# Optimization experiments

Hardware: AMD Instinct MI355X
Metric: run time of the kernel (lower is better)

The kernel has to match this reference:

```python
import jax, jax.numpy as jnp
import numpy as np

ALPHA = 0.1

def setup_inputs() -> dict:
    key = jax.random.key(0)
    k1, k2, k3, k4 = jax.random.split(key, 4)
    B, T, D_IN, H, R = 32, 2048, 128, 512, 2
    x = jax.random.normal(k1, (B, T, D_IN), dtype=jnp.float32)
    m = jax.random.normal(k2, (H, R), dtype=jnp.float32) / np.sqrt(H)
    n = jax.random.normal(k3, (H, R), dtype=jnp.float32) / np.sqrt(H)
    I = jax.random.normal(k4, (H, D_IN), dtype=jnp.float32) / np.sqrt(H)
    return {"x": x, "m": m, "n": n, "I": I}

def reference(x, m, n, I):
    # x: [B, T, D_in]; m,n: [H, R]; I: [H, D_in]
    B = x.shape[0]
    H = m.shape[0]
    J = m @ n.T  # [H, H] low-rank recurrent matrix, as in the torch module
    # Precompute input projection for all timesteps: (I @ x_t^T)^T == x_t @ I^T
    x_proj = jnp.einsum('btd,hd->bth', x, I)  # [B, T, H]
    h0 = jnp.zeros((B, H), dtype=x.dtype)

    def step(h, xp_t):
        dh = -h + jnp.tanh(h) @ J.T + xp_t  # (J @ tanh(h)^T)^T == tanh(h) @ J^T
        h = h + ALPHA * dh
        return h, h

    _, hiddens = jax.lax.scan(step, h0, jnp.swapaxes(x_proj, 0, 1))  # [T, B, H]
    return jnp.swapaxes(hiddens, 0, 1)  # [B, T, H]
```

## Files before the change

### kernel.cpp

```cpp
#include <hip/hip_runtime.h>


#define ALPHA 0.1f
typedef float v2 __attribute__((ext_vector_type(2)));
typedef short s16x8 __attribute__((ext_vector_type(8)));
typedef float f32x4 __attribute__((ext_vector_type(4)));
typedef unsigned short u16x8 __attribute__((ext_vector_type(8)));
typedef __attribute__((address_space(1))) ushort g_u16;
typedef __attribute__((address_space(3))) ushort l_u16;

__device__ __forceinline__ ushort f2bf(float x) {
  uint u = __float_as_uint(x);
  return (ushort)((u + 0x7FFFu + ((u >> 16) & 1u)) >> 16);
}
__device__ __forceinline__ float bf2f(ushort h) {
  return __uint_as_float(((uint)h) << 16);
}
__device__ __forceinline__ int swz(int row, int k) {
  return row * 128 + (k ^ ((row & 7) << 3));
}

#define MFMA __builtin_amdgcn_mfma_f32_16x16x32_bf16

__global__ __launch_bounds__(256)
void to_bf16_swz(const float* __restrict__ X, const float* __restrict__ Iw,
                 ushort* __restrict__ Xh, ushort* __restrict__ Ih) {
  const int b = blockIdx.x;
  const float* src;
  ushort* dh;
  int gid;
  if (b < 4096) {
    src = X; dh = Xh; gid = b * 256 + threadIdx.x;
  } else {
    src = Iw; dh = Ih; gid = (b - 4096) * 256 + threadIdx.x;
  }
  const int row = gid >> 4;
  const int k0 = (gid & 15) * 8;
  const float4* p = (const float4*)(src + (size_t)row * 128 + k0);
  float4 a = p[0], bq = p[1];
  float v[8] = {a.x, a.y, a.z, a.w, bq.x, bq.y, bq.z, bq.w};
  u16x8 hi;
#pragma unroll
  for (int i = 0; i < 8; ++i) hi[i] = f2bf(v[i]);
  const int ks = k0 ^ ((row & 7) << 3);
  *(u16x8*)&dh[(size_t)row * 128 + ks] = hi;
}

__global__ __launch_bounds__(256, 4)
void xproj_gemm2(const ushort* __restrict__ Xh, const ushort* __restrict__ Ih,
                 ushort* __restrict__ C) {
  __shared__ ushort Ahs[64 * 128];
  __shared__ ushort Bhs[64 * 128];

  const int u = blockIdx.x;
  const int m0 = ((u & 7) * 128 + (u >> 6)) * 64;
  const int n0 = ((u >> 3) & 7) * 64;

  const int id = threadIdx.x;
  const int lane = id & 63;
  const int wid = id >> 6;

  {
    const int half = (wid & 1) * 32;
    const ushort* g;
    ushort* l;
    if (wid < 2) { g = Xh + (size_t)(m0 + half) * 128; l = Ahs + half * 128; }
    else         { g = Ih + (size_t)(n0 + half) * 128; l = Bhs + half * 128; }
    g += lane * 8;
#pragma unroll
    for (int i = 0; i < 8; ++i)
      __builtin_amdgcn_global_load_lds((const g_u16*)(g + i * 512),
                                       (l_u16*)(l + i * 512), 16, 0, 0);
  }
  __syncthreads();

  const int wr = (wid >> 1) * 32;
  const int wc = (wid & 1) * 32;
  const int fr = lane & 15;
  const int fk = (lane >> 4) * 8;

  f32x4 acc[2][2] = {};

#pragma unroll
  for (int kk = 0; kk < 4; ++kk) {
    const int kb = kk * 32 + fk;
    s16x8 ahi[2], bhi[2];
#pragma unroll
    for (int i = 0; i < 2; ++i)
      ahi[i] = *(const s16x8*)&Ahs[swz(wr + i * 16 + fr, kb)];
#pragma unroll
    for (int jn = 0; jn < 2; ++jn)
      bhi[jn] = *(const s16x8*)&Bhs[swz(wc + jn * 16 + fr, kb)];
#pragma unroll
    for (int i = 0; i < 2; ++i)
#pragma unroll
      for (int jn = 0; jn < 2; ++jn)
        acc[i][jn] = MFMA(ahi[i], bhi[jn], acc[i][jn], 0, 0, 0);
  }

#pragma unroll
  for (int i = 0; i < 2; ++i)
#pragma unroll
    for (int jn = 0; jn < 2; ++jn) {
      int r0 = m0 + wr + i * 16 + (lane >> 4) * 4;
      int c0 = n0 + wc + jn * 16 + (lane & 15);
#pragma unroll
      for (int t = 0; t < 4; ++t)
        C[(size_t)(r0 + t) * 512 + c0] = f2bf(acc[i][jn][t]);
    }
}

__global__ __launch_bounds__(256, 2)
void xproj_gemm_fused(const float* __restrict__ X, const float* __restrict__ Iw,
                      float* __restrict__ C) {
  __shared__ ushort Ahs[64 * 128];
  __shared__ ushort Bhs[64 * 128];

  const int u = blockIdx.x;
  const int m0 = ((u & 7) * 128 + (u >> 6)) * 64;
  const int n0 = ((u >> 3) & 7) * 64;
  const int id = threadIdx.x;

#pragma unroll
  for (int j = 0; j < 8; ++j) {
    int f = id + 256 * j;
    int row = f >> 5, c4 = f & 31;
    int k0 = 4 * c4;
    float4 a4 = *(const float4*)(X + (size_t)(m0 + row) * 128 + k0);
    float4 b4 = *(const float4*)(Iw + (size_t)(n0 + row) * 128 + k0);
    int sa = swz(row, k0);
    *(ushort4*)&Ahs[sa] =
        make_ushort4(f2bf(a4.x), f2bf(a4.y), f2bf(a4.z), f2bf(a4.w));
    *(ushort4*)&Bhs[sa] =
        make_ushort4(f2bf(b4.x), f2bf(b4.y), f2bf(b4.z), f2bf(b4.w));
  }
  __syncthreads();

  const int lane = id & 63;
  const int wid = id >> 6;
  const int wr = (wid >> 1) * 32;
  const int wc = (wid & 1) * 32;
  const int fr = lane & 15;
  const int fk = (lane >> 4) * 8;

  f32x4 acc[2][2] = {};
#pragma unroll
  for (int kk = 0; kk < 4; ++kk) {
    const int kb = kk * 32 + fk;
    s16x8 ahi[2], bhi[2];
#pragma unroll
    for (int i = 0; i < 2; ++i)
      ahi[i] = *(const s16x8*)&Ahs[swz(wr + i * 16 + fr, kb)];
#pragma unroll
    for (int jn = 0; jn < 2; ++jn)
      bhi[jn] = *(const s16x8*)&Bhs[swz(wc + jn * 16 + fr, kb)];
#pragma unroll
    for (int i = 0; i < 2; ++i)
#pragma unroll
      for (int jn = 0; jn < 2; ++jn)
        acc[i][jn] = MFMA(ahi[i], bhi[jn], acc[i][jn], 0, 0, 0);
  }
#pragma unroll
  for (int i = 0; i < 2; ++i)
#pragma unroll
    for (int jn = 0; jn < 2; ++jn) {
      int r0 = m0 + wr + i * 16 + (lane >> 4) * 4;
      int c0 = n0 + wc + jn * 16 + (lane & 15);
#pragma unroll
      for (int t = 0; t < 4; ++t)
        C[(size_t)(r0 + t) * 512 + c0] = acc[i][jn][t];
    }
}

#define DPP_STEP(v, ctrl)                                                     \
  ((v) + __int_as_float(__builtin_amdgcn_update_dpp(                          \
             0, __float_as_int(v), (ctrl), 0xf, 0xf, true)))

__device__ __forceinline__ float wave_sum63(float v) {
  v = DPP_STEP(v, 0x111);
  v = DPP_STEP(v, 0x112);
  v = DPP_STEP(v, 0x114);
  v = DPP_STEP(v, 0x118);
  v = DPP_STEP(v, 0x142);
  v = DPP_STEP(v, 0x143);
  return v;
}

struct ScanState {
  v2 m0v[4], m1v[4], n0v[4], n1v[4], hv[4];
};

__device__ __forceinline__ void scan_init(ScanState& S, const float* mw,
                                          const float* nw, int base) {
  const float2* mp = (const float2*)mw;
  const float2* np = (const float2*)nw;
#pragma unroll
  for (int p = 0; p < 4; ++p) {
    float2 ma = mp[base + 2 * p], mb = mp[base + 2 * p + 1];
    float2 na = np[base + 2 * p], nb = np[base + 2 * p + 1];
    S.m0v[p] = (v2){ma.x, mb.x};
    S.m1v[p] = (v2){ma.y, mb.y};
    S.n0v[p] = (v2){ALPHA * na.x, ALPHA * nb.x};
    S.n1v[p] = (v2){ALPHA * na.y, ALPHA * nb.y};
    S.hv[p] = (v2){0.f, 0.f};
  }
}

__device__ __forceinline__ void scan_step(ScanState& S, u16x8 xr) {
  const v2 TC0 = (v2){-5.70498872745e-3f, -5.70498872745e-3f};
  const v2 TC1 = (v2){2.06390887954e-2f, 2.06390887954e-2f};
  const v2 TC2 = (v2){-5.37397155531e-2f, -5.37397155531e-2f};
  const v2 TC3 = (v2){1.33314422036e-1f, 1.33314422036e-1f};
  const v2 TC4 = (v2){-3.33332819422e-1f, -3.33332819422e-1f};
  const v2 CLO = (v2){-1.15f, -1.15f};
  const v2 CHI = (v2){1.15f, 1.15f};
  const v2 K9 = (v2){1.f - ALPHA, 1.f - ALPHA};
  const v2 KA = (v2){ALPHA, ALPHA};

  v2 xpv[4];
#pragma unroll
  for (int p = 0; p < 4; ++p)
    xpv[p] = (v2){bf2f(xr[2 * p]), bf2f(xr[2 * p + 1])};

  v2 p0 = (v2){0.f, 0.f}, p1 = (v2){0.f, 0.f};
#pragma unroll
  for (int p = 0; p < 4; ++p) {
    v2 xc = __builtin_elementwise_min(
        __builtin_elementwise_max(S.hv[p], CLO), CHI);
    v2 z = xc * xc;
    v2 q = __builtin_elementwise_fma(z, TC0, TC1);
    q = __builtin_elementwise_fma(z, q, TC2);
    q = __builtin_elementwise_fma(z, q, TC3);
    q = __builtin_elementwise_fma(z, q, TC4);
    v2 th = __builtin_elementwise_fma(xc * z, q, xc);
    p0 = __builtin_elementwise_fma(th, S.n0v[p], p0);
    p1 = __builtin_elementwise_fma(th, S.n1v[p], p1);
  }
  float s0 = wave_sum63(p0.x + p0.y);
  float s1 = wave_sum63(p1.x + p1.y);
  s0 = __int_as_float(__builtin_amdgcn_readlane(__float_as_int(s0), 63));
  s1 = __int_as_float(__builtin_amdgcn_readlane(__float_as_int(s1), 63));
  v2 s0v = (v2){s0, s0}, s1v = (v2){s1, s1};
#pragma unroll
  for (int p = 0; p < 4; ++p) {
    v2 d = __builtin_elementwise_fma(s0v, S.m0v[p], s1v * S.m1v[p]);
    S.hv[p] = __builtin_elementwise_fma(
        K9, S.hv[p], __builtin_elementwise_fma(KA, xpv[p], d));
  }
}

#define CS 32
#define CW 96

__global__ __launch_bounds__(64, 1)
void rnn_scan_chunk(const float* __restrict__ mw, const float* __restrict__ nw,
                    const ushort* __restrict__ xp, float* __restrict__ out) {
  const int b = blockIdx.x;
  const int c = blockIdx.y;
  const int base = threadIdx.x * 8;

  ScanState S;
  scan_init(S, mw, nw, base);

  const ushort* xrow = xp + (size_t)b * 2048 * 512 + base;
  float* orow = out + (size_t)b * 2048 * 512 + base;

  const int t1 = c * CS;
  int t0 = t1 - CW;
  if (t0 < 0) t0 = 0;
  const int t2 = t1 + CS;
  const int warm_blocks = (t1 - t0) >> 3;
  const int tot_blocks = (t2 - t0) >> 3;

  u16x8 ra[8];
#pragma unroll
  for (int u = 0; u < 8; ++u)
    ra[u] = *(const u16x8*)(xrow + (size_t)(t0 + u) * 512);

  for (int bb = 0; bb < tot_blocks; ++bb) {
    const int tb = t0 + bb * 8;
    const bool refill = (bb + 1 < tot_blocks);
    const bool dostore = (bb >= warm_blocks);
#pragma unroll
    for (int u = 0; u < 8; ++u) {
      u16x8 xr = ra[u];
      if (refill)
        ra[u] = *(const u16x8*)(xrow + (size_t)(tb + 8 + u) * 512);
      scan_step(S, xr);
      if (dostore) {
        f32x4 o0 = {S.hv[0].x, S.hv[0].y, S.hv[1].x, S.hv[1].y};
        f32x4 o1 = {S.hv[2].x, S.hv[2].y, S.hv[3].x, S.hv[3].y};
        __builtin_nontemporal_store(o0, (f32x4*)(orow + (size_t)(tb + u) * 512));
        __builtin_nontemporal_store(o1, (f32x4*)(orow + (size_t)(tb + u) * 512 + 4));
      }
    }
  }
}

__device__ __forceinline__ void scan_step_f32(ScanState& S, float4 xa, float4 xb) {
  u16x8 dummy;
  const v2 TC0 = (v2){-5.70498872745e-3f, -5.70498872745e-3f};
  const v2 TC1 = (v2){2.06390887954e-2f, 2.06390887954e-2f};
  const v2 TC2 = (v2){-5.37397155531e-2f, -5.37397155531e-2f};
  const v2 TC3 = (v2){1.33314422036e-1f, 1.33314422036e-1f};
  const v2 TC4 = (v2){-3.33332819422e-1f, -3.33332819422e-1f};
  const v2 CLO = (v2){-1.15f, -1.15f};
  const v2 CHI = (v2){1.15f, 1.15f};
  const v2 K9 = (v2){1.f - ALPHA, 1.f - ALPHA};
  const v2 KA = (v2){ALPHA, ALPHA};
  (void)dummy;
  v2 xpv[4] = {(v2){xa.x, xa.y}, (v2){xa.z, xa.w},
               (v2){xb.x, xb.y}, (v2){xb.z, xb.w}};
  v2 p0 = (v2){0.f, 0.f}, p1 = (v2){0.f, 0.f};
#pragma unroll
  for (int p = 0; p < 4; ++p) {
    v2 xc = __builtin_elementwise_min(
        __builtin_elementwise_max(S.hv[p], CLO), CHI);
    v2 z = xc * xc;
    v2 q = __builtin_elementwise_fma(z, TC0, TC1);
    q = __builtin_elementwise_fma(z, q, TC2);
    q = __builtin_elementwise_fma(z, q, TC3);
    q = __builtin_elementwise_fma(z, q, TC4);
    v2 th = __builtin_elementwise_fma(xc * z, q, xc);
    p0 = __builtin_elementwise_fma(th, S.n0v[p], p0);
    p1 = __builtin_elementwise_fma(th, S.n1v[p], p1);
  }
  float s0 = wave_sum63(p0.x + p0.y);
  float s1 = wave_sum63(p1.x + p1.y);
  s0 = __int_as_float(__builtin_amdgcn_readlane(__float_as_int(s0), 63));
  s1 = __int_as_float(__builtin_amdgcn_readlane(__float_as_int(s1), 63));
  v2 s0v = (v2){s0, s0}, s1v = (v2){s1, s1};
#pragma unroll
  for (int p = 0; p < 4; ++p) {
    v2 d = __builtin_elementwise_fma(s0v, S.m0v[p], s1v * S.m1v[p]);
    S.hv[p] = __builtin_elementwise_fma(
        K9, S.hv[p], __builtin_elementwise_fma(KA, xpv[p], d));
  }
}

__global__ __launch_bounds__(64, 1)
void rnn_scan_serial(const float* __restrict__ mw, const float* __restrict__ nw,
                     float* __restrict__ out) {
  const int b = blockIdx.x;
  const int base = threadIdx.x * 8;
  ScanState S;
  scan_init(S, mw, nw, base);
  float* row = out + (size_t)b * 2048 * 512 + base;

  float4 ra[8], rb[8];
#pragma unroll
  for (int u = 0; u < 8; ++u) {
    ra[u] = *(const float4*)(row + (size_t)u * 512);
    rb[u] = *(const float4*)(row + (size_t)u * 512 + 4);
  }
  for (int bb = 0; bb < 256; ++bb) {
    const int tb = bb * 8;
    const bool refill = (bb + 1 < 256);
#pragma unroll
    for (int u = 0; u < 8; ++u) {
      float4 xa = ra[u], xb = rb[u];
      if (refill) {
        ra[u] = *(const float4*)(row + (size_t)(tb + 8 + u) * 512);
        rb[u] = *(const float4*)(row + (size_t)(tb + 8 + u) * 512 + 4);
      }
      scan_step_f32(S, xa, xb);
      *(float4*)(row + (size_t)(tb + u) * 512) =
          make_float4(S.hv[0].x, S.hv[0].y, S.hv[1].x, S.hv[1].y);
      *(float4*)(row + (size_t)(tb + u) * 512 + 4) =
          make_float4(S.hv[2].x, S.hv[2].y, S.hv[3].x, S.hv[3].y);
    }
  }
}

extern "C" void kernel_launch(void* const* d_in, const int* in_sizes, int n_in,
                              void* d_out, int out_size, void* d_ws, size_t ws_size,
                              hipStream_t stream) {
  const float* x  = (const float*)d_in[0];
  const float* mw = (const float*)d_in[1];
  const float* nw = (const float*)d_in[2];
  const float* Iw = (const float*)d_in[3];
  float* out = (float*)d_out;

  const size_t xp_bytes = 32ull * 2048ull * 512ull * 2ull;

  if (ws_size >= xp_bytes) {
    ushort* xp = (ushort*)d_ws;
    ushort* Xh = (ushort*)out;
    ushort* Ih = Xh + 65536ull * 128ull;
    to_bf16_swz<<<4128, 256, 0, stream>>>(x, Iw, Xh, Ih);
    xproj_gemm2<<<8192, 256, 0, stream>>>(Xh, Ih, xp);
    rnn_scan_chunk<<<dim3(32, 2048 / CS), 64, 0, stream>>>(mw, nw, xp, out);
  } else {
    xproj_gemm_fused<<<8192, 256, 0, stream>>>(x, Iw, out);
    rnn_scan_serial<<<32, 64, 0, stream>>>(mw, nw, out);
  }
}
```

Baseline: 242.3 us.

## Interleave two independent scan chunks per wave to hide serial latency

Each 64-thread block now processes two adjacent time chunks, A and B, of the same batch row in lockstep. Their independent recurrences are interleaved so the DPP reduction and tanh-polynomial latency of one chain can overlap with the other, and the grid shrinks from 64 to 32 chunk-blocks per batch. The cost is double the register state and fewer waves in flight. Chunk A runs fewer steps than chunk B and is masked off for its last blocks, but it still executes those redundant steps.

Result: slower. 278.0 us (+14.7%).

```diff
diff --git a/kernel.cpp b/kernel.cpp
--- a/kernel.cpp
+++ b/kernel.cpp
@@ -186,12 +186,12 @@
   return v;
 }
 
-struct ScanState {
-  v2 m0v[4], m1v[4], n0v[4], n1v[4], hv[4];
+struct ScanState2 {
+  v2 m0v[4], m1v[4], n0v[4], n1v[4], hA[4], hB[4];
 };
 
-__device__ __forceinline__ void scan_init(ScanState& S, const float* mw,
-                                          const float* nw, int base) {
+__device__ __forceinline__ void scan_init2(ScanState2& S, const float* mw,
+                                           const float* nw, int base) {
   const float2* mp = (const float2*)mw;
   const float2* np = (const float2*)nw;
 #pragma unroll
@@ -202,11 +202,12 @@
     S.m1v[p] = (v2){ma.y, mb.y};
     S.n0v[p] = (v2){ALPHA * na.x, ALPHA * nb.x};
     S.n1v[p] = (v2){ALPHA * na.y, ALPHA * nb.y};
-    S.hv[p] = (v2){0.f, 0.f};
-  }
-}
-
-__device__ __forceinline__ void scan_step(ScanState& S, u16x8 xr) {
+    S.hA[p] = (v2){0.f, 0.f};
+    S.hB[p] = (v2){0.f, 0.f};
+  }
+}
+
+__device__ __forceinline__ void scan_step2(ScanState2& S, u16x8 xrA, u16x8 xrB) {
   const v2 TC0 = (v2){-5.70498872745e-3f, -5.70498872745e-3f};
   const v2 TC1 = (v2){2.06390887954e-2f, 2.06390887954e-2f};
   const v2 TC2 = (v2){-5.37397155531e-2f, -5.37397155531e-2f};
@@ -217,35 +218,55 @@
   const v2 K9 = (v2){1.f - ALPHA, 1.f - ALPHA};
   const v2 KA = (v2){ALPHA, ALPHA};
 
-  v2 xpv[4];
-#pragma unroll
-  for (int p = 0; p < 4; ++p)
-    xpv[p] = (v2){bf2f(xr[2 * p]), bf2f(xr[2 * p + 1])};
-
-  v2 p0 = (v2){0.f, 0.f}, p1 = (v2){0.f, 0.f};
-#pragma unroll
-  for (int p = 0; p < 4; ++p) {
-    v2 xc = __builtin_elementwise_min(
-        __builtin_elementwise_max(S.hv[p], CLO), CHI);
-    v2 z = xc * xc;
-    v2 q = __builtin_elementwise_fma(z, TC0, TC1);
-    q = __builtin_elementwise_fma(z, q, TC2);
-    q = __builtin_elementwise_fma(z, q, TC3);
-    q = __builtin_elementwise_fma(z, q, TC4);
-    v2 th = __builtin_elementwise_fma(xc * z, q, xc);
-    p0 = __builtin_elementwise_fma(th, S.n0v[p], p0);
-    p1 = __builtin_elementwise_fma(th, S.n1v[p], p1);
-  }
-  float s0 = wave_sum63(p0.x + p0.y);
-  float s1 = wave_sum63(p1.x + p1.y);
-  s0 = __int_as_float(__builtin_amdgcn_readlane(__float_as_int(s0), 63));
-  s1 = __int_as_float(__builtin_amdgcn_readlane(__float_as_int(s1), 63));
-  v2 s0v = (v2){s0, s0}, s1v = (v2){s1, s1};
-#pragma unroll
-  for (int p = 0; p < 4; ++p) {
-    v2 d = __builtin_elementwise_fma(s0v, S.m0v[p], s1v * S.m1v[p]);
-    S.hv[p] = __builtin_elementwise_fma(
-        K9, S.hv[p], __builtin_elementwise_fma(KA, xpv[p], d));
+  v2 xpA[4], xpB[4];
+#pragma unroll
+  for (int p = 0; p < 4; ++p) {
+    xpA[p] = (v2){bf2f(xrA[2 * p]), bf2f(xrA[2 * p + 1])};
+    xpB[p] = (v2){bf2f(xrB[2 * p]), bf2f(xrB[2 * p + 1])};
+  }
+
+  v2 p0A = (v2){0.f, 0.f}, p1A = (v2){0.f, 0.f};
+  v2 p0B = (v2){0.f, 0.f}, p1B = (v2){0.f, 0.f};
+#pragma unroll
+  for (int p = 0; p < 4; ++p) {
+    v2 xcA = __builtin_elementwise_min(
+        __builtin_elementwise_max(S.hA[p], CLO), CHI);
+    v2 xcB = __builtin_elementwise_min(
+        __builtin_elementwise_max(S.hB[p], CLO), CHI);
+    v2 zA = xcA * xcA, zB = xcB * xcB;
+    v2 qA = __builtin_elementwise_fma(zA, TC0, TC1);
+    v2 qB = __builtin_elementwise_fma(zB, TC0, TC1);
+    qA = __builtin_elementwise_fma(zA, qA, TC2);
+    qB = __builtin_elementwise_fma(zB, qB, TC2);
+    qA = __builtin_elementwise_fma(zA, qA, TC3);
+    qB = __builtin_elementwise_fma(zB, qB, TC3);
+    qA = __builtin_elementwise_fma(zA, qA, TC4);
+    qB = __builtin_elementwise_fma(zB, qB, TC4);
+    v2 thA = __builtin_elementwise_fma(xcA * zA, qA, xcA);
+    v2 thB = __builtin_elementwise_fma(xcB * zB, qB, xcB);
+    p0A = __builtin_elementwise_fma(thA, S.n0v[p], p0A);
+    p1A = __builtin_elementwise_fma(thA, S.n1v[p], p1A);
+    p0B = __builtin_elementwise_fma(thB, S.n0v[p], p0B);
+    p1B = __builtin_elementwise_fma(thB, S.n1v[p], p1B);
+  }
+  float s0A = wave_sum63(p0A.x + p0A.y);
+  float s1A = wave_sum63(p1A.x + p1A.y);
+  float s0B = wave_sum63(p0B.x + p0B.y);
+  float s1B = wave_sum63(p1B.x + p1B.y);
+  s0A = __int_as_float(__builtin_amdgcn_readlane(__float_as_int(s0A), 63));
+  s1A = __int_as_float(__builtin_amdgcn_readlane(__float_as_int(s1A), 63));
+  s0B = __int_as_float(__builtin_amdgcn_readlane(__float_as_int(s0B), 63));
+  s1B = __int_as_float(__builtin_amdgcn_readlane(__float_as_int(s1B), 63));
+  v2 s0Av = (v2){s0A, s0A}, s1Av = (v2){s1A, s1A};
+  v2 s0Bv = (v2){s0B, s0B}, s1Bv = (v2){s1B, s1B};
+#pragma unroll
+  for (int p = 0; p < 4; ++p) {
+    v2 dA = __builtin_elementwise_fma(s0Av, S.m0v[p], s1Av * S.m1v[p]);
+    v2 dB = __builtin_elementwise_fma(s0Bv, S.m0v[p], s1Bv * S.m1v[p]);
+    S.hA[p] = __builtin_elementwise_fma(
+        K9, S.hA[p], __builtin_elementwise_fma(KA, xpA[p], dA));
+    S.hB[p] = __builtin_elementwise_fma(
+        K9, S.hB[p], __builtin_elementwise_fma(KA, xpB[p], dB));
   }
 }
 
@@ -256,49 +277,75 @@
 void rnn_scan_chunk(const float* __restrict__ mw, const float* __restrict__ nw,
                     const ushort* __restrict__ xp, float* __restrict__ out) {
   const int b = blockIdx.x;
-  const int c = blockIdx.y;
+  const int cA = blockIdx.y * 2, cB = cA + 1;
   const int base = threadIdx.x * 8;
 
-  ScanState S;
-  scan_init(S, mw, nw, base);
+  ScanState2 S;
+  scan_init2(S, mw, nw, base);
 
   const ushort* xrow = xp + (size_t)b * 2048 * 512 + base;
   float* orow = out + (size_t)b * 2048 * 512 + base;
 
-  const int t1 = c * CS;
-  int t0 = t1 - CW;
-  if (t0 < 0) t0 = 0;
-  const int t2 = t1 + CS;
-  const int warm_blocks = (t1 - t0) >> 3;
-  const int tot_blocks = (t2 - t0) >> 3;
-
-  u16x8 ra[8];
-#pragma unroll
-  for (int u = 0; u < 8; ++u)
-    ra[u] = *(const u16x8*)(xrow + (size_t)(t0 + u) * 512);
-
-  for (int bb = 0; bb < tot_blocks; ++bb) {
-    const int tb = t0 + bb * 8;
-    const bool refill = (bb + 1 < tot_blocks);
-    const bool dostore = (bb >= warm_blocks);
+  const int t1A = cA * CS, t1B = cB * CS;
+  const int t0A = (t1A < CW) ? 0 : t1A - CW;
+  const int t0B = (t1B < CW) ? 0 : t1B - CW;
+  const int warmA = (t1A - t0A) >> 3, totA = (t1A + CS - t0A) >> 3;
+  const int warmB = (t1B - t0B) >> 3, totB = (t1B + CS - t0B) >> 3;
+
+  u16x8 raA[8], raB[8];
+#pragma unroll
+  for (int u = 0; u < 8; ++u) {
+    raA[u] = *(const u16x8*)(xrow + (size_t)(t0A + u) * 512);
+    raB[u] = *(const u16x8*)(xrow + (size_t)(t0B + u) * 512);
+  }
+
+  for (int bb = 0; bb < totB; ++bb) {
+    const int tbA = t0A + bb * 8, tbB = t0B + bb * 8;
+    const bool refA = (bb + 1 < totA), refB = (bb + 1 < totB);
+    const bool stA = (bb >= warmA) && (bb < totA), stB = (bb >= warmB);
 #pragma unroll
     for (int u = 0; u < 8; ++u) {
-      u16x8 xr = ra[u];
-      if (refill)
-        ra[u] = *(const u16x8*)(xrow + (size_t)(tb + 8 + u) * 512);
-      scan_step(S, xr);
-      if (dostore) {
-        f32x4 o0 = {S.hv[0].x, S.hv[0].y, S.hv[1].x, S.hv[1].y};
-        f32x4 o1 = {S.hv[2].x, S.hv[2].y, S.hv[3].x, S.hv[3].y};
-        __builtin_nontemporal_store(o0, (f32x4*)(orow + (size_t)(tb + u) * 512));
-        __builtin_nontemporal_store(o1, (f32x4*)(orow + (size_t)(tb + u) * 512 + 4));
+      u16x8 xrA = raA[u], xrB = raB[u];
+      if (refA) raA[u] = *(const u16x8*)(xrow + (size_t)(tbA + 8 + u) * 512);
+      if (refB) raB[u] = *(const u16x8*)(xrow + (size_t)(tbB + 8 + u) * 512);
+      scan_step2(S, xrA, xrB);
+      if (stA) {
+        f32x4 o0 = {S.hA[0].x, S.hA[0].y, S.hA[1].x, S.hA[1].y};
+        f32x4 o1 = {S.hA[2].x, S.hA[2].y, S.hA[3].x, S.hA[3].y};
+        __builtin_nontemporal_store(o0, (f32x4*)(orow + (size_t)(tbA + u) * 512));
+        __builtin_nontemporal_store(o1, (f32x4*)(orow + (size_t)(tbA + u) * 512 + 4));
+      }
+      if (stB) {
+        f32x4 o0 = {S.hB[0].x, S.hB[0].y, S.hB[1].x, S.hB[1].y};
+        f32x4 o1 = {S.hB[2].x, S.hB[2].y, S.hB[3].x, S.hB[3].y};
+        __builtin_nontemporal_store(o0, (f32x4*)(orow + (size_t)(tbB + u) * 512));
+        __builtin_nontemporal_store(o1, (f32x4*)(orow + (size_t)(tbB + u) * 512 + 4));
       }
     }
   }
 }
 
+struct ScanState {
+  v2 m0v[4], m1v[4], n0v[4], n1v[4], hv[4];
+};
+
+__device__ __forceinline__ void scan_init(ScanState& S, const float* mw,
+                                          const float* nw, int base) {
+  const float2* mp = (const float2*)mw;
+  const float2* np = (const float2*)nw;
+#pragma unroll
+  for (int p = 0; p < 4; ++p) {
+    float2 ma = mp[base + 2 * p], mb = mp[base + 2 * p + 1];
+    float2 na = np[base + 2 * p], nb = np[base + 2 * p + 1];
+    S.m0v[p] = (v2){ma.x, mb.x};
+    S.m1v[p] = (v2){ma.y, mb.y};
+    S.n0v[p] = (v2){ALPHA * na.x, ALPHA * nb.x};
+    S.n1v[p] = (v2){ALPHA * na.y, ALPHA * nb.y};
+    S.hv[p] = (v2){0.f, 0.f};
+  }
+}
+
 __device__ __forceinline__ void scan_step_f32(ScanState& S, float4 xa, float4 xb) {
-  u16x8 dummy;
   const v2 TC0 = (v2){-5.70498872745e-3f, -5.70498872745e-3f};
   const v2 TC1 = (v2){2.06390887954e-2f, 2.06390887954e-2f};
   const v2 TC2 = (v2){-5.37397155531e-2f, -5.37397155531e-2f};
@@ -308,7 +355,6 @@
   const v2 CHI = (v2){1.15f, 1.15f};
   const v2 K9 = (v2){1.f - ALPHA, 1.f - ALPHA};
   const v2 KA = (v2){ALPHA, ALPHA};
-  (void)dummy;
   v2 xpv[4] = {(v2){xa.x, xa.y}, (v2){xa.z, xa.w},
                (v2){xb.x, xb.y}, (v2){xb.z, xb.w}};
   v2 p0 = (v2){0.f, 0.f}, p1 = (v2){0.f, 0.f};
@@ -389,7 +435,7 @@
     ushort* Ih = Xh + 65536ull * 128ull;
     to_bf16_swz<<<4128, 256, 0, stream>>>(x, Iw, Xh, Ih);
     xproj_gemm2<<<8192, 256, 0, stream>>>(Xh, Ih, xp);
-    rnn_scan_chunk<<<dim3(32, 2048 / CS), 64, 0, stream>>>(mw, nw, xp, out);
+    rnn_scan_chunk<<<dim3(32, 32), 64, 0, stream>>>(mw, nw, xp, out);
   } else {
     xproj_gemm_fused<<<8192, 256, 0, stream>>>(x, Iw, out);
     rnn_scan_serial<<<32, 64, 0, stream>>>(mw, nw, out);
```
